# Performance work log

Measured on AMD Instinct MI355X. Metric: run time of the kernel, lower is better.

Reference implementation:

```python
import jax, jax.numpy as jnp
import numpy as np

L, B, E, H, NH = 128, 32, 128, 256, 8
NUM_NODE, ETA = 20000, 100


def setup_inputs() -> dict:
    key = jax.random.key(0)
    ks = jax.random.split(key, 24)
    s = 0.05
    rn = lambda k, sh: jax.random.normal(k, sh, dtype=jnp.float32) * s
    return {
        "node": jax.random.randint(ks[0], (L, B), 0, NUM_NODE + 1),
        "ts": jax.random.normal(ks[1], (L, B, 2), dtype=jnp.float32),
        "seq_lengths": jnp.sort(jax.random.randint(ks[2], (B,), 64, L + 1))[::-1],
        "embed_table": rn(ks[3], (NUM_NODE + 1, E)),
        "Wih0": rn(ks[4], (3 * H, E + 2)), "Whh0": rn(ks[5], (3 * H, H)),
        "bih0": rn(ks[6], (3 * H,)), "bhh0": rn(ks[7], (3 * H,)),
        "Wih1": rn(ks[8], (3 * H, H)), "Whh1": rn(ks[9], (3 * H, H)),
        "bih1": rn(ks[10], (3 * H,)), "bhh1": rn(ks[11], (3 * H,)),
        "Wa0": rn(ks[12], (E, 2 * E)), "ba0": rn(ks[13], (E,)),
        "Wa1": rn(ks[14], (NH, E)), "ba1": rn(ks[15], (NH,)),
        "Wf0": rn(ks[16], (168, H * (NH + 1))), "bf0": rn(ks[17], (168,)),
        "Wf1": rn(ks[18], (ETA, 168)), "bf1": rn(ks[19], (ETA,)),
    }


def gru_layer(x, Wih, Whh, bih, bhh, lengths):
    # x: [L, B, in]; PyTorch GRU cell, with pack/pad semantics:
    # hidden frozen and output zeroed for t >= length (emulates pack_padded_sequence).
    Lx, Bx, _ = x.shape

    def step(h, xs):
        x_t, t = xs
        gi = x_t @ Wih.T + bih          # [B, 3H]
        gh = h @ Whh.T + bhh            # [B, 3H]
        ir, iz, in_ = jnp.split(gi, 3, axis=-1)
        hr, hz, hn = jnp.split(gh, 3, axis=-1)
        r = jax.nn.sigmoid(ir + hr)
        z = jax.nn.sigmoid(iz + hz)
        n = jnp.tanh(in_ + r * hn)
        h_new = (1.0 - z) * n + z * h
        valid = (t < lengths)[:, None]
        h = jnp.where(valid, h_new, h)
        return h, jnp.where(valid, h_new, jnp.zeros_like(h_new))

    h0 = jnp.zeros((Bx, Whh.shape[1]), x.dtype)
    hT, outs = jax.lax.scan(step, h0, (x, jnp.arange(Lx)))
    return outs, hT


def reference(node, ts, seq_lengths, embed_table,
              Wih0, Whh0, bih0, bhh0, Wih1, Whh1, bih1, bhh1,
              Wa0, ba0, Wa1, ba1, Wf0, bf0, Wf1, bf1):
    e = embed_table[node]                          # [L, B, E]
    embeds = jnp.concatenate([e, ts], axis=-1)     # [L, B, E+2]

    # pairwise attention: a[i,j] = e[j], b[i,j] = e[i] (repeat + transpose)
    a = jnp.broadcast_to(e[None], (L, L, B, E))
    b = jnp.broadcast_to(e[:, None], (L, L, B, E))
    pair = jnp.concatenate([a, b], axis=-1)        # [L, L, B, 2E]
    hid = jax.nn.relu(pair @ Wa0.T + ba0)          # [L, L, B, E]
    w = (hid @ Wa1.T + ba1).sum(axis=1)            # [L, B, NH]

    # multiplicative length mask, then softmax over time axis (as in original)
    mask = (jnp.arange(L)[:, None] < seq_lengths[None, :]).astype(w.dtype)[..., None]
    w = jax.nn.softmax(w * mask, axis=0)           # [L, B, NH]

    out0, _ = gru_layer(embeds, Wih0, Whh0, bih0, bhh0, seq_lengths)
    out1, hT = gru_layer(out0, Wih1, Whh1, bih1, bhh1, seq_lengths)  # [L,B,H], [B,H]

    ctx = jnp.einsum('lbh,lbd->bhd', w, out1).reshape(B, NH * H)     # [B, NH*H]
    z = jnp.concatenate([ctx, hT], axis=-1) @ Wf0.T + bf0
    z = jax.nn.selu(z)
    logits = z @ Wf1.T + bf1
    return jax.nn.log_softmax(logits, axis=-1)
```

## Files before the change

### kernel.cpp

```cpp
#include <hip/hip_runtime.h>
#include <hip/hip_bf16.h>
#include <hip/hip_fp8.h>

#define LL 128
#define BB 32
#define EE 128
#define HH 256
#define NHH 8
#define G3 768
#define IN0 130
#define ETA 100
#define F1 168
#define CLSIN 2304

typedef _Float16 half_t;
typedef __attribute__((ext_vector_type(2))) _Float16 half2v;
typedef __attribute__((ext_vector_type(4))) float floatx4;

#if defined(__has_builtin)
#if __has_builtin(__builtin_amdgcn_fdot2)
#define HAVE_FDOT2 1
#endif
#endif

__device__ __forceinline__ float fdot2f(half2v a, half2v b, float c) {
#ifdef HAVE_FDOT2
  return __builtin_amdgcn_fdot2(a, b, c, false);
#else
  return c + (float)a.x * (float)b.x + (float)a.y * (float)b.y;
#endif
}

#define BARRIER_LDS() __asm__ volatile("s_waitcnt lgkmcnt(0)\n\ts_barrier" ::: "memory")

__device__ __forceinline__ float sigmoidf_(float x) { return 1.0f / (1.0f + __expf(-x)); }
__device__ __forceinline__ float tanhf_(float x) { return 1.0f - 2.0f / (__expf(2.0f * x) + 1.0f); }

__global__ void prep_kernel(
    const float* __restrict__ Wa0, const float* __restrict__ Wih0,
    const float* __restrict__ Wih1, const float* __restrict__ Whh0,
    const float* __restrict__ Whh1,
    half_t* __restrict__ Wa0Ta, half_t* __restrict__ Wa0Tb,
    half2v* __restrict__ Wih0T2, half2v* __restrict__ Wih1T2,
    __hip_fp8_e4m3* __restrict__ Whh0q, __hip_fp8_e4m3* __restrict__ Whh1q)
{
  int idx = blockIdx.x * blockDim.x + threadIdx.x;
  const int n1 = 16384, n2 = 16384, n3 = 65 * 768, n4 = 128 * 768, n5 = 196608;
  if (idx < n1) {
    int d = idx >> 7, k = idx & 127;
    Wa0Ta[idx] = (half_t)Wa0[k * 256 + d];
  } else if ((idx -= n1) < n2) {
    int d = idx >> 7, k = idx & 127;
    Wa0Tb[idx] = (half_t)Wa0[k * 256 + 128 + d];
  } else if ((idx -= n2) < n3) {
    int d2 = idx / 768, r = idx % 768;
    half2v w; w.x = (half_t)Wih0[r * IN0 + 2 * d2]; w.y = (half_t)Wih0[r * IN0 + 2 * d2 + 1];
    Wih0T2[idx] = w;
  } else if ((idx -= n3) < n4) {
    int d2 = idx / 768, r = idx % 768;
    half2v w; w.x = (half_t)Wih1[r * HH + 2 * d2]; w.y = (half_t)Wih1[r * HH + 2 * d2 + 1];
    Wih1T2[idx] = w;
  } else if ((idx -= n4) < n5) {
    Whh0q[idx] = __hip_fp8_e4m3(Whh0[idx]);
  } else if ((idx -= n5) < n5) {
    Whh1q[idx] = __hip_fp8_e4m3(Whh1[idx]);
  }
}

__global__ void embed_uv_kernel(
    const int* __restrict__ node,
    const float* __restrict__ table,
    const half_t* __restrict__ Wa0Ta,
    const half_t* __restrict__ Wa0Tb,
    const float* __restrict__ ba0,
    half2v* __restrict__ e_h2,
    float* __restrict__ U,
    float* __restrict__ V)
{
  int lb = blockIdx.x;
  int k = threadIdx.x;
  __shared__ float es[EE];
  int n = node[lb];
  float ev = table[(size_t)n * EE + k];
  es[k] = ev;
  __syncthreads();
  if (k < 64) {
    half2v p; p.x = (half_t)es[2 * k]; p.y = (half_t)es[2 * k + 1];
    e_h2[(size_t)lb * 64 + k] = p;
  }
  float u = 0.f, v = ba0[k];
  #pragma unroll 8
  for (int d = 0; d < EE; ++d) {
    float x = es[d];
    u += (float)Wa0Ta[d * EE + k] * x;
    v += (float)Wa0Tb[d * EE + k] * x;
  }
  U[(size_t)lb * EE + k] = u;
  V[(size_t)lb * EE + k] = v;
}

__global__ __launch_bounds__(128) void attn_w_kernel(
    const float* __restrict__ U, const float* __restrict__ V,
    const float* __restrict__ Wa1,
    const float* __restrict__ ba1,
    float* __restrict__ wpre)
{
  int ig = blockIdx.x >> 5;
  int b = blockIdx.x & 31;
  int i0 = ig * 4;
  int k = threadIdx.x;
  float vk[4];
  #pragma unroll
  for (int ii = 0; ii < 4; ++ii) vk[ii] = V[((size_t)(i0 + ii) * BB + b) * EE + k];
  float wa[NHH], acc[4][NHH];
  #pragma unroll
  for (int h = 0; h < NHH; ++h) wa[h] = Wa1[h * EE + k];
  #pragma unroll
  for (int ii = 0; ii < 4; ++ii)
    #pragma unroll
    for (int h = 0; h < NHH; ++h) acc[ii][h] = 0.f;
  for (int j = 0; j < LL; ++j) {
    float u = U[((size_t)j * BB + b) * EE + k];
    #pragma unroll
    for (int ii = 0; ii < 4; ++ii) {
      float tv = fmaxf(u + vk[ii], 0.f);
      #pragma unroll
      for (int h = 0; h < NHH; ++h) acc[ii][h] += wa[h] * tv;
    }
  }
  __shared__ float part[2][32];
  int wave = k >> 6, lane = k & 63;
  #pragma unroll
  for (int ii = 0; ii < 4; ++ii)
    #pragma unroll
    for (int h = 0; h < NHH; ++h) {
      float a = acc[ii][h];
      #pragma unroll
      for (int off = 32; off > 0; off >>= 1) a += __shfl_xor(a, off, 64);
      if (lane == 0) part[wave][ii * 8 + h] = a;
    }
  __syncthreads();
  if (k < 32) {
    int ii = k >> 3, h = k & 7;
    float w = part[0][k] + part[1][k] + (float)LL * ba1[h];
    wpre[((size_t)(i0 + ii) * BB + b) * NHH + h] = w;
  }
}

__global__ void attn_softmax_kernel(
    const float* __restrict__ wpre, const int* __restrict__ slen,
    float* __restrict__ wsoft)
{
  int b = blockIdx.x >> 3;
  int h = blockIdx.x & 7;
  int l = threadIdx.x;
  int len = slen[b];
  float x = wpre[((size_t)l * BB + b) * NHH + h];
  float xv = (l < len) ? x : 0.f;
  float m = xv;
  #pragma unroll
  for (int off = 32; off > 0; off >>= 1) m = fmaxf(m, __shfl_xor(m, off, 64));
  __shared__ float sm[2], ss[2];
  int wave = l >> 6;
  if ((l & 63) == 0) sm[wave] = m;
  __syncthreads();
  m = fmaxf(sm[0], sm[1]);
  float e = __expf(xv - m);
  float s = e;
  #pragma unroll
  for (int off = 32; off > 0; off >>= 1) s += __shfl_xor(s, off, 64);
  if ((l & 63) == 0) ss[wave] = s;
  __syncthreads();
  s = ss[0] + ss[1];
  wsoft[((size_t)l * BB + b) * NHH + h] = e / s;
}

__global__ __launch_bounds__(256) void gi0_kernel(
    const half2v* __restrict__ e_h2, const float* __restrict__ ts,
    const half2v* __restrict__ W2,
    const float* __restrict__ bih,
    float* __restrict__ gi)
{
  int lb0 = blockIdx.x * 8;
  int tid = threadIdx.x;
  __shared__ half2v xs2[8][66];
  for (int idx = tid; idx < 512; idx += 256) {
    int q = idx >> 6, d2 = idx & 63;
    xs2[q][d2] = e_h2[(size_t)(lb0 + q) * 64 + d2];
  }
  if (tid < 8) {
    half2v t2; t2.x = (half_t)ts[(lb0 + tid) * 2]; t2.y = (half_t)ts[(lb0 + tid) * 2 + 1];
    xs2[tid][64] = t2;
  }
  __syncthreads();
  float acc[8][3];
  #pragma unroll
  for (int q = 0; q < 8; ++q) { acc[q][0] = 0.f; acc[q][1] = 0.f; acc[q][2] = 0.f; }
  for (int d2 = 0; d2 < 65; ++d2) {
    half2v w0 = W2[d2 * 768 + tid];
    half2v w1 = W2[d2 * 768 + 256 + tid];
    half2v w2 = W2[d2 * 768 + 512 + tid];
    #pragma unroll
    for (int q = 0; q < 8; ++q) {
      half2v x = xs2[q][d2];
      acc[q][0] = fdot2f(w0, x, acc[q][0]);
      acc[q][1] = fdot2f(w1, x, acc[q][1]);
      acc[q][2] = fdot2f(w2, x, acc[q][2]);
    }
  }
  float b0 = bih[tid], b1 = bih[256 + tid], b2 = bih[512 + tid];
  #pragma unroll
  for (int q = 0; q < 8; ++q) {
    float* gp = gi + (size_t)(lb0 + q) * G3;
    gp[tid] = acc[q][0] + b0; gp[256 + tid] = acc[q][1] + b1; gp[512 + tid] = acc[q][2] + b2;
  }
}

__global__ __launch_bounds__(256) void gi1_kernel(
    const float* __restrict__ out0,
    const half2v* __restrict__ W2,
    const float* __restrict__ bih,
    float* __restrict__ gi)
{
  int lb0 = blockIdx.x * 8;
  int tid = threadIdx.x;
  __shared__ half2v xs2[8][128];
  for (int idx = tid; idx < 1024; idx += 256) {
    int q = idx >> 7, d2 = idx & 127;
    float2 v = ((const float2*)(out0 + (size_t)(lb0 + q) * HH))[d2];
    half2v x; x.x = (half_t)v.x; x.y = (half_t)v.y;
    xs2[q][d2] = x;
  }
  __syncthreads();
  float acc[8][3];
  #pragma unroll
  for (int q = 0; q < 8; ++q) { acc[q][0] = 0.f; acc[q][1] = 0.f; acc[q][2] = 0.f; }
  for (int d2 = 0; d2 < 128; ++d2) {
    half2v w0 = W2[d2 * 768 + tid];
    half2v w1 = W2[d2 * 768 + 256 + tid];
    half2v w2 = W2[d2 * 768 + 512 + tid];
    #pragma unroll
    for (int q = 0; q < 8; ++q) {
      half2v x = xs2[q][d2];
      acc[q][0] = fdot2f(w0, x, acc[q][0]);
      acc[q][1] = fdot2f(w1, x, acc[q][1]);
      acc[q][2] = fdot2f(w2, x, acc[q][2]);
    }
  }
  float b0 = bih[tid], b1 = bih[256 + tid], b2 = bih[512 + tid];
  #pragma unroll
  for (int q = 0; q < 8; ++q) {
    float* gp = gi + (size_t)(lb0 + q) * G3;
    gp[tid] = acc[q][0] + b0; gp[256 + tid] = acc[q][1] + b1; gp[512 + tid] = acc[q][2] + b2;
  }
}

__global__ __launch_bounds__(256, 1) void gru_scan_kernel(
    const __hip_fp8_e4m3* __restrict__ Whhq,
    const float* __restrict__ bhh,
    const float* __restrict__ gi,
    const int* __restrict__ slen,
    float* __restrict__ out,
    float* __restrict__ hT)
{
  const int b = blockIdx.x;
  const int tid = threadIdx.x;
  const int w = tid >> 6;
  const int lane = tid & 63;
  const int col = lane & 15;
  const int quad = lane >> 4;
  __shared__ __align__(16) unsigned char hs[HH];

  const unsigned char* Wq = (const unsigned char*)Whhq;

  uint2 wf[96];
  #pragma unroll
  for (int g3 = 0; g3 < 3; ++g3) {
    #pragma unroll
    for (int tau = 0; tau < 4; ++tau) {
      int row = 256 * g3 + 64 * w + 16 * tau + col;
      const uint2* rp = (const uint2*)(Wq + (size_t)row * HH + 8 * quad);
      #pragma unroll
      for (int ks = 0; ks < 8; ++ks)
        wf[(g3 * 4 + tau) * 8 + ks] = rp[ks * 4];
    }
  }

  const int len = slen[b];
  float hold[4], br[4], bz[4], bn[4];
  #pragma unroll
  for (int tau = 0; tau < 4; ++tau) {
    int j = 64 * w + 16 * tau + col;
    hold[tau] = 0.f;
    br[tau] = bhh[j]; bz[tau] = bhh[256 + j]; bn[tau] = bhh[512 + j];
  }
  if (tid < 64) ((unsigned int*)hs)[tid] = 0u;
  __syncthreads();

  const float* gib = gi + (size_t)b * G3;
  float* outb = out + (size_t)b * HH;

  float c0[4], c1[4], c2[4];
  #pragma unroll
  for (int tau = 0; tau < 4; ++tau) {
    int j = 64 * w + 16 * tau + col;
    c0[tau] = gib[j]; c1[tau] = gib[256 + j]; c2[tau] = gib[512 + j];
  }

  #pragma unroll 1
  for (int t = 0; t < LL; ++t) {
    int t2 = (t + 1 < LL) ? (t + 1) : t;
    const float* gq = gib + (size_t)t2 * (BB * G3);
    float n0[4], n1[4], n2[4];
    #pragma unroll
    for (int tau = 0; tau < 4; ++tau) {
      int j = 64 * w + 16 * tau + col;
      n0[tau] = gq[j]; n1[tau] = gq[256 + j]; n2[tau] = gq[512 + j];
    }
    floatx4 acc[12];
    #pragma unroll
    for (int i = 0; i < 12; ++i) { floatx4 z = {0.f, 0.f, 0.f, 0.f}; acc[i] = z; }
    #pragma unroll
    for (int ks = 0; ks < 8; ++ks) {
      uint2 hf = *(const uint2*)(hs + 32 * ks + 8 * quad);
      long ha = __builtin_bit_cast(long, hf);
      #pragma unroll
      for (int tt = 0; tt < 12; ++tt)
        acc[tt] = __builtin_amdgcn_mfma_f32_16x16x32_fp8_fp8(
            ha, __builtin_bit_cast(long, wf[tt * 8 + ks]), acc[tt], 0, 0, 0);
    }
    BARRIER_LDS();
    bool valid = t < len;
    #pragma unroll
    for (int tau = 0; tau < 4; ++tau) {
      float r_ = sigmoidf_(c0[tau] + acc[tau].x + br[tau]);
      float z_ = sigmoidf_(c1[tau] + acc[4 + tau].x + bz[tau]);
      float nn = tanhf_(c2[tau] + r_ * (acc[8 + tau].x + bn[tau]));
      float hnew = (1.f - z_) * nn + z_ * hold[tau];
      hold[tau] = valid ? hnew : hold[tau];
      if (lane < 16) {
        int j = 64 * w + 16 * tau + col;
        ((__hip_fp8_e4m3*)hs)[j] = __hip_fp8_e4m3(hold[tau]);
        outb[(size_t)t * (BB * HH) + j] = valid ? hnew : 0.f;
      }
      c0[tau] = n0[tau]; c1[tau] = n1[tau]; c2[tau] = n2[tau];
    }
    BARRIER_LDS();
  }
  if (lane < 16) {
    #pragma unroll
    for (int tau = 0; tau < 4; ++tau)
      hT[(size_t)b * HH + 64 * w + 16 * tau + col] = hold[tau];
  }
}

__global__ void ctx_kernel(
    const float* __restrict__ wsoft, const float* __restrict__ out1,
    float* __restrict__ ctx)
{
  int b = blockIdx.x >> 3, h = blockIdx.x & 7;
  int d = threadIdx.x;
  float acc = 0.f;
  for (int l = 0; l < LL; ++l) {
    float w = wsoft[((size_t)l * BB + b) * NHH + h];
    acc += w * out1[((size_t)l * BB + b) * HH + d];
  }
  ctx[(size_t)b * (NHH * HH) + h * HH + d] = acc;
}

__global__ __launch_bounds__(512) void final_kernel(
    const float* __restrict__ ctx, const float* __restrict__ hT,
    const float* __restrict__ Wf0,
    const float* __restrict__ bf0,
    const float* __restrict__ Wf1,
    const float* __restrict__ bf1,
    float* __restrict__ outp)
{
  int b = blockIdx.x;
  int tid = threadIdx.x;
  int wave = tid >> 6, lane = tid & 63;
  __shared__ float4 xs4[CLSIN / 4];
  __shared__ float zs[F1];
  __shared__ float ls[ETA];
  float* xs = (float*)xs4;
  for (int i = tid; i < NHH * HH; i += 512) xs[i] = ctx[(size_t)b * (NHH * HH) + i];
  if (tid < HH) xs[NHH * HH + tid] = hT[(size_t)b * HH + tid];
  __syncthreads();
  for (int r = wave; r < F1; r += 8) {
    const float4* wp = (const float4*)(Wf0 + (size_t)r * CLSIN);
    float acc = 0.f;
    #pragma unroll
    for (int i = 0; i < CLSIN / 4 / 64; ++i) {
      float4 w = wp[lane + 64 * i];
      float4 x = xs4[lane + 64 * i];
      acc += w.x * x.x + w.y * x.y + w.z * x.z + w.w * x.w;
    }
    #pragma unroll
    for (int off = 32; off > 0; off >>= 1) acc += __shfl_xor(acc, off, 64);
    if (lane == 0) {
      float x = acc + bf0[r];
      const float alpha = 1.6732632423543772f, scale = 1.0507009873554805f;
      zs[r] = scale * (x > 0.f ? x : alpha * (__expf(x) - 1.f));
    }
  }
  __syncthreads();
  for (int r = wave; r < ETA; r += 8) {
    float acc = 0.f;
    for (int k = lane; k < F1; k += 64) acc += Wf1[r * F1 + k] * zs[k];
    #pragma unroll
    for (int off = 32; off > 0; off >>= 1) acc += __shfl_xor(acc, off, 64);
    if (lane == 0) ls[r] = acc + bf1[r];
  }
  __syncthreads();
  if (wave == 0) {
    float v0 = (lane < ETA) ? ls[lane] : -1e30f;
    float v1 = (lane + 64 < ETA) ? ls[lane + 64] : -1e30f;
    float m = fmaxf(v0, v1);
    #pragma unroll
    for (int off = 32; off > 0; off >>= 1) m = fmaxf(m, __shfl_xor(m, off, 64));
    float s = __expf(v0 - m) + __expf(v1 - m);
    #pragma unroll
    for (int off = 32; off > 0; off >>= 1) s += __shfl_xor(s, off, 64);
    float lse = m + __logf(s);
    if (lane < ETA) outp[(size_t)b * ETA + lane] = v0 - lse;
    if (lane + 64 < ETA) outp[(size_t)b * ETA + lane + 64] = v1 - lse;
  }
}

extern "C" void kernel_launch(void* const* d_in, const int* in_sizes, int n_in,
                              void* d_out, int out_size, void* d_ws, size_t ws_size,
                              hipStream_t stream) {
  const int*   node  = (const int*)d_in[0];
  const float* ts    = (const float*)d_in[1];
  const int*   slen  = (const int*)d_in[2];
  const float* table = (const float*)d_in[3];
  const float* Wih0  = (const float*)d_in[4];
  const float* Whh0  = (const float*)d_in[5];
  const float* bih0  = (const float*)d_in[6];
  const float* bhh0  = (const float*)d_in[7];
  const float* Wih1  = (const float*)d_in[8];
  const float* Whh1  = (const float*)d_in[9];
  const float* bih1  = (const float*)d_in[10];
  const float* bhh1  = (const float*)d_in[11];
  const float* Wa0   = (const float*)d_in[12];
  const float* ba0   = (const float*)d_in[13];
  const float* Wa1   = (const float*)d_in[14];
  const float* ba1   = (const float*)d_in[15];
  const float* Wf0   = (const float*)d_in[16];
  const float* bf0   = (const float*)d_in[17];
  const float* Wf1   = (const float*)d_in[18];
  const float* bf1   = (const float*)d_in[19];

  char* ws = (char*)d_ws;
  size_t off = 0;
  auto alloc = [&](size_t n) { void* p = (void*)(ws + off); off += (n + 255) & ~(size_t)255; return p; };

  half2v* e_h2 = (half2v*)alloc((size_t)LL * BB * 64 * 4);
  float* U     = (float*)alloc((size_t)LL * BB * EE * 4);
  float* V     = (float*)alloc((size_t)LL * BB * EE * 4);
  float* gi    = (float*)alloc((size_t)LL * BB * G3 * 4);
  float* out0  = (float*)alloc((size_t)LL * BB * HH * 4);
  float* out1  = (float*)alloc((size_t)LL * BB * HH * 4);
  float* hTb   = (float*)alloc((size_t)BB * HH * 4);
  float* wpre  = (float*)alloc((size_t)LL * BB * NHH * 4);
  float* wsoft = (float*)alloc((size_t)LL * BB * NHH * 4);
  float* ctxb  = (float*)alloc((size_t)BB * NHH * HH * 4);
  half_t* Wa0Ta = (half_t*)alloc((size_t)128 * 128 * 2);
  half_t* Wa0Tb = (half_t*)alloc((size_t)128 * 128 * 2);
  half2v* Wih0T2 = (half2v*)alloc((size_t)65 * 768 * 4);
  half2v* Wih1T2 = (half2v*)alloc((size_t)128 * 768 * 4);
  __hip_fp8_e4m3* Whh0q = (__hip_fp8_e4m3*)alloc((size_t)G3 * HH);
  __hip_fp8_e4m3* Whh1q = (__hip_fp8_e4m3*)alloc((size_t)G3 * HH);
  if (off > ws_size) return;

  const int prep_total = 16384 + 16384 + 65 * 768 + 128 * 768 + 196608 + 196608;
  prep_kernel<<<(prep_total + 255) / 256, 256, 0, stream>>>(
      Wa0, Wih0, Wih1, Whh0, Whh1, Wa0Ta, Wa0Tb, Wih0T2, Wih1T2, Whh0q, Whh1q);
  embed_uv_kernel<<<LL * BB, 128, 0, stream>>>(node, table, Wa0Ta, Wa0Tb, ba0, e_h2, U, V);
  attn_w_kernel<<<(LL / 4) * BB, 128, 0, stream>>>(U, V, Wa1, ba1, wpre);
  attn_softmax_kernel<<<BB * NHH, 128, 0, stream>>>(wpre, slen, wsoft);
  gi0_kernel<<<LL * BB / 8, 256, 0, stream>>>(e_h2, ts, Wih0T2, bih0, gi);
  gru_scan_kernel<<<BB, 256, 0, stream>>>(Whh0q, bhh0, gi, slen, out0, hTb);
  gi1_kernel<<<LL * BB / 8, 256, 0, stream>>>(out0, Wih1T2, bih1, gi);
  gru_scan_kernel<<<BB, 256, 0, stream>>>(Whh1q, bhh1, gi, slen, out1, hTb);
  ctx_kernel<<<BB * NHH, 256, 0, stream>>>(wsoft, out1, ctxb);
  final_kernel<<<BB, 512, 0, stream>>>(ctxb, hTb, Wf0, bf0, Wf1, bf1, (float*)d_out);
}
```

Measured before the change: 694.5 us.

## Stream GRU recurrent weights from cache per step, double-buffer hidden state, fuse ctx into final

The GRU scan kernel no longer keeps the whole fp8 Whh fragment set (96 uint2) in registers. Each step now reloads it from global/L2 in four rotating groups that overlap with the MFMA groups, which cuts register pressure at the cost of extra memory traffic every step. The hidden state in LDS is double-buffered, which removes one barrier per step. The context einsum kernel is folded into the final classifier kernel, dropping a launch and an intermediate buffer.

```diff
diff --git a/kernel.cpp b/kernel.cpp
--- a/kernel.cpp
+++ b/kernel.cpp
@@ -269,21 +269,31 @@
   const int lane = tid & 63;
   const int col = lane & 15;
   const int quad = lane >> 4;
-  __shared__ __align__(16) unsigned char hs[HH];
+  __shared__ __align__(8) unsigned char hs[2][HH];
 
   const unsigned char* Wq = (const unsigned char*)Whhq;
-
-  uint2 wf[96];
-  #pragma unroll
-  for (int g3 = 0; g3 < 3; ++g3) {
-    #pragma unroll
-    for (int tau = 0; tau < 4; ++tau) {
-      int row = 256 * g3 + 64 * w + 16 * tau + col;
-      const uint2* rp = (const uint2*)(Wq + (size_t)row * HH + 8 * quad);
-      #pragma unroll
-      for (int ks = 0; ks < 8; ++ks)
-        wf[(g3 * 4 + tau) * 8 + ks] = rp[ks * 4];
-    }
+  const unsigned char* base = Wq + (size_t)(64 * w + col) * HH + 8 * quad;
+#define TOFF(tt) (((tt) >> 2) * 65536 + ((tt) & 3) * 4096)
+
+  uint2 wbuf[4][24];
+#define LOADG(g)                                                            \
+  {                                                                         \
+    _Pragma("unroll")                                                       \
+    for (int i = 0; i < 24; ++i) {                                          \
+      int tt = (g) * 3 + (i >> 3);                                          \
+      wbuf[g][i] = *(const uint2*)(base + TOFF(tt) + (i & 7) * 32);         \
+    }                                                                       \
+  }
+#define MFMAG(g)                                                            \
+  {                                                                         \
+    _Pragma("unroll")                                                       \
+    for (int ks = 0; ks < 8; ++ks) {                                        \
+      _Pragma("unroll")                                                     \
+      for (int j = 0; j < 3; ++j)                                           \
+        acc[(g) * 3 + j] = __builtin_amdgcn_mfma_f32_16x16x32_fp8_fp8(      \
+            ha[ks], __builtin_bit_cast(long, wbuf[g][j * 8 + ks]),          \
+            acc[(g) * 3 + j], 0, 0, 0);                                     \
+    }                                                                       \
   }
 
   const int len = slen[b];
@@ -294,42 +304,40 @@
     hold[tau] = 0.f;
     br[tau] = bhh[j]; bz[tau] = bhh[256 + j]; bn[tau] = bhh[512 + j];
   }
-  if (tid < 64) ((unsigned int*)hs)[tid] = 0u;
+  if (tid < 128) ((unsigned int*)hs)[tid] = 0u;
   __syncthreads();
 
   const float* gib = gi + (size_t)b * G3;
   float* outb = out + (size_t)b * HH;
 
-  float c0[4], c1[4], c2[4];
-  #pragma unroll
-  for (int tau = 0; tau < 4; ++tau) {
-    int j = 64 * w + 16 * tau + col;
-    c0[tau] = gib[j]; c1[tau] = gib[256 + j]; c2[tau] = gib[512 + j];
-  }
+  LOADG(0)
 
   #pragma unroll 1
   for (int t = 0; t < LL; ++t) {
-    int t2 = (t + 1 < LL) ? (t + 1) : t;
-    const float* gq = gib + (size_t)t2 * (BB * G3);
-    float n0[4], n1[4], n2[4];
+    const unsigned char* hr = hs[t & 1];
+    unsigned char* hw = (unsigned char*)hs[(t & 1) ^ 1];
+    LOADG(1)
+    const float* gp = gib + (size_t)t * (BB * G3);
+    float c0[4], c1[4], c2[4];
     #pragma unroll
     for (int tau = 0; tau < 4; ++tau) {
       int j = 64 * w + 16 * tau + col;
-      n0[tau] = gq[j]; n1[tau] = gq[256 + j]; n2[tau] = gq[512 + j];
-    }
+      c0[tau] = gp[j]; c1[tau] = gp[256 + j]; c2[tau] = gp[512 + j];
+    }
+    long ha[8];
+    #pragma unroll
+    for (int ks = 0; ks < 8; ++ks)
+      ha[ks] = __builtin_bit_cast(long, *(const uint2*)(hr + 32 * ks + 8 * quad));
     floatx4 acc[12];
     #pragma unroll
     for (int i = 0; i < 12; ++i) { floatx4 z = {0.f, 0.f, 0.f, 0.f}; acc[i] = z; }
-    #pragma unroll
-    for (int ks = 0; ks < 8; ++ks) {
-      uint2 hf = *(const uint2*)(hs + 32 * ks + 8 * quad);
-      long ha = __builtin_bit_cast(long, hf);
-      #pragma unroll
-      for (int tt = 0; tt < 12; ++tt)
-        acc[tt] = __builtin_amdgcn_mfma_f32_16x16x32_fp8_fp8(
-            ha, __builtin_bit_cast(long, wf[tt * 8 + ks]), acc[tt], 0, 0, 0);
-    }
-    BARRIER_LDS();
+    MFMAG(0)
+    LOADG(2)
+    MFMAG(1)
+    LOADG(3)
+    MFMAG(2)
+    LOADG(0)
+    MFMAG(3)
     bool valid = t < len;
     #pragma unroll
     for (int tau = 0; tau < 4; ++tau) {
@@ -340,10 +348,9 @@
       hold[tau] = valid ? hnew : hold[tau];
       if (lane < 16) {
         int j = 64 * w + 16 * tau + col;
-        ((__hip_fp8_e4m3*)hs)[j] = __hip_fp8_e4m3(hold[tau]);
+        ((__hip_fp8_e4m3*)hw)[j] = __hip_fp8_e4m3(hold[tau]);
         outb[(size_t)t * (BB * HH) + j] = valid ? hnew : 0.f;
       }
-      c0[tau] = n0[tau]; c1[tau] = n1[tau]; c2[tau] = n2[tau];
     }
     BARRIER_LDS();
   }
@@ -352,24 +359,15 @@
     for (int tau = 0; tau < 4; ++tau)
       hT[(size_t)b * HH + 64 * w + 16 * tau + col] = hold[tau];
   }
-}
-
-__global__ void ctx_kernel(
-    const float* __restrict__ wsoft, const float* __restrict__ out1,
-    float* __restrict__ ctx)
-{
-  int b = blockIdx.x >> 3, h = blockIdx.x & 7;
-  int d = threadIdx.x;
-  float acc = 0.f;
-  for (int l = 0; l < LL; ++l) {
-    float w = wsoft[((size_t)l * BB + b) * NHH + h];
-    acc += w * out1[((size_t)l * BB + b) * HH + d];
-  }
-  ctx[(size_t)b * (NHH * HH) + h * HH + d] = acc;
+#undef LOADG
+#undef MFMAG
+#undef TOFF
 }
 
 __global__ __launch_bounds__(512) void final_kernel(
-    const float* __restrict__ ctx, const float* __restrict__ hT,
+    const float* __restrict__ wsoft,
+    const float* __restrict__ out1,
+    const float* __restrict__ hT,
     const float* __restrict__ Wf0,
     const float* __restrict__ bf0,
     const float* __restrict__ Wf1,
@@ -380,12 +378,36 @@
   int tid = threadIdx.x;
   int wave = tid >> 6, lane = tid & 63;
   __shared__ float4 xs4[CLSIN / 4];
+  __shared__ float ws[LL][NHH];
+  __shared__ float part[NHH * HH];
   __shared__ float zs[F1];
   __shared__ float ls[ETA];
   float* xs = (float*)xs4;
-  for (int i = tid; i < NHH * HH; i += 512) xs[i] = ctx[(size_t)b * (NHH * HH) + i];
+  for (int i = tid; i < LL * NHH; i += 512) {
+    int l = i >> 3, h = i & 7;
+    ws[l][h] = wsoft[((size_t)l * BB + b) * NHH + h];
+  }
   if (tid < HH) xs[NHH * HH + tid] = hT[(size_t)b * HH + tid];
   __syncthreads();
+  {
+    int d = tid & 255, lh = tid >> 8;
+    float ac[NHH] = {0.f, 0.f, 0.f, 0.f, 0.f, 0.f, 0.f, 0.f};
+    for (int l = 64 * lh; l < 64 * (lh + 1); ++l) {
+      float x = out1[((size_t)l * BB + b) * HH + d];
+      #pragma unroll
+      for (int h = 0; h < NHH; ++h) ac[h] += ws[l][h] * x;
+    }
+    if (lh) {
+      #pragma unroll
+      for (int h = 0; h < NHH; ++h) part[h * HH + d] = ac[h];
+    }
+    __syncthreads();
+    if (!lh) {
+      #pragma unroll
+      for (int h = 0; h < NHH; ++h) xs[h * HH + d] = ac[h] + part[h * HH + d];
+    }
+    __syncthreads();
+  }
   for (int r = wave; r < F1; r += 8) {
     const float4* wp = (const float4*)(Wf0 + (size_t)r * CLSIN);
     float acc = 0.f;
@@ -464,7 +486,6 @@
   float* hTb   = (float*)alloc((size_t)BB * HH * 4);
   float* wpre  = (float*)alloc((size_t)LL * BB * NHH * 4);
   float* wsoft = (float*)alloc((size_t)LL * BB * NHH * 4);
-  float* ctxb  = (float*)alloc((size_t)BB * NHH * HH * 4);
   half_t* Wa0Ta = (half_t*)alloc((size_t)128 * 128 * 2);
   half_t* Wa0Tb = (half_t*)alloc((size_t)128 * 128 * 2);
   half2v* Wih0T2 = (half2v*)alloc((size_t)65 * 768 * 4);
@@ -483,6 +504,5 @@
   gru_scan_kernel<<<BB, 256, 0, stream>>>(Whh0q, bhh0, gi, slen, out0, hTb);
   gi1_kernel<<<LL * BB / 8, 256, 0, stream>>>(out0, Wih1T2, bih1, gi);
   gru_scan_kernel<<<BB, 256, 0, stream>>>(Whh1q, bhh1, gi, slen, out1, hTb);
-  ctx_kernel<<<BB * NHH, 256, 0, stream>>>(wsoft, out1, ctxb);
-  final_kernel<<<BB, 512, 0, stream>>>(ctxb, hTb, Wf0, bf0, Wf1, bf1, (float*)d_out);
-}
+  final_kernel<<<BB, 512, 0, stream>>>(wsoft, out1, hTb, Wf0, bf0, Wf1, bf1, (float*)d_out);
+}
```

Result: faster. 665.4 us (-4.2%).
